# Optimization experiments

Measured on AMD Instinct MI355X. Metric: run time of the kernel, lower is better.

## Reference

```python
import jax, jax.numpy as jnp
import numpy as np
import math

N_HEADS = 8
EMB = 128
KEY_DIM = EMB // N_HEADS  # 16
B, NQ, T = 32, 1024, 1024


def _uniform(key, shape, stdv):
    return jax.random.uniform(key, shape, jnp.float32, -stdv, stdv)


def setup_inputs() -> dict:
    key = jax.random.key(0)
    ks = jax.random.split(key, 7)
    stdv = 1.0 / math.sqrt(KEY_DIM)      # last dim of w_query/w_key/w_value
    stdv_o = 1.0 / math.sqrt(EMB)        # last dim of w_out
    q = jax.random.normal(ks[0], (B, NQ, EMB), jnp.float32)
    h = jax.random.normal(ks[1], (B, T, EMB), jnp.float32)
    mask = jax.random.randint(ks[2], (B, NQ, T), 0, 2).astype(bool)
    return {
        "q": q,
        "h": h,
        "mask": mask,
        "w_query": _uniform(ks[3], (N_HEADS, EMB, KEY_DIM), stdv),
        "w_key": _uniform(ks[4], (N_HEADS, EMB, KEY_DIM), stdv),
        "w_value": _uniform(ks[5], (N_HEADS, EMB, KEY_DIM), stdv),
        "w_out": _uniform(ks[6], (N_HEADS, KEY_DIM, EMB), stdv_o),
    }


def reference(q, h, mask, w_query, w_key, w_value, w_out):
    # q: [B, NQ, E], h: [B, T, E], mask: [B, NQ, T] (True = blocked)
    scale = 1.0 / math.sqrt(KEY_DIM)
    Q = jnp.einsum('bqi,hik->hbqk', q, w_query)   # [H,B,NQ,dk]
    K = jnp.einsum('bti,hik->hbtk', h, w_key)     # [H,B,T,dk]
    V = jnp.einsum('bti,hiv->hbtv', h, w_value)   # [H,B,T,dv]
    U = scale * jnp.einsum('hbqk,hbtk->hbqt', Q, K)  # [H,B,NQ,T]
    m = mask[None]                                   # broadcast over heads
    U = jnp.where(m, -jnp.inf, U)
    attn = jax.nn.softmax(U, axis=-1)
    attn = jnp.where(m, 0.0, attn)                   # explicit zeroing as in original
    heads = jnp.einsum('hbqt,hbtv->hbqv', attn, V)   # [H,B,NQ,dv]
    out = jnp.einsum('hbqv,hve->bqe', heads, w_out)  # [B,NQ,E]
    return out
```

## Files before the change

kernel.cpp:

```cpp
#include <hip/hip_runtime.h>
#include <hip/hip_bf16.h>
#include <stdint.h>


typedef __attribute__((ext_vector_type(8))) short bf16x8;
typedef __attribute__((ext_vector_type(4))) float f32x4;
typedef __attribute__((ext_vector_type(16))) float f32x16;

#define NEGBIG (-1e30f)
#define QSCALE 0.36067376022224085f
#define EXP2(x) __builtin_amdgcn_exp2f(x)
#define PSTRIDE 68

__device__ __forceinline__ unsigned short f2bf(float x) {
  union { __hip_bfloat16 h; unsigned short u; } cv;
  cv.h = __float2bfloat16(x);
  return cv.u;
}
__device__ __forceinline__ unsigned int pk2bf(float a, float b) {
  unsigned int ua = __float_as_uint(a) + 0x8000u;
  unsigned int ub = __float_as_uint(b) + 0x8000u;
  return __builtin_amdgcn_perm(ub, ua, 0x07060302u);
}
__device__ __forceinline__ unsigned int pk2bf_t(float a, float b) {
  return __builtin_amdgcn_perm(__float_as_uint(b), __float_as_uint(a), 0x07060302u);
}

__global__ __launch_bounds__(256) void projmask_k(const float* __restrict__ qp,
                                                  const float* __restrict__ hp,
                                                  const float* __restrict__ wqp,
                                                  const float* __restrict__ wkp,
                                                  const float* __restrict__ wvp,
                                                  const void* __restrict__ mask,
                                                  unsigned short* __restrict__ Qb,
                                                  unsigned short* __restrict__ Kb,
                                                  unsigned short* __restrict__ Vt,
                                                  unsigned long long* __restrict__ mp64) {
  __shared__ unsigned short WtLds[128 * 136];
  __shared__ __align__(16) unsigned short Cxf[9216];
  const int tid = threadIdx.x;

  if (blockIdx.x >= 1536) {
    const int bx = blockIdx.x - 1536;
    unsigned short* mlds = WtLds;
    const unsigned int* mi = (const unsigned int*)mask;
    unsigned int accv = 0;
    #pragma unroll
    for (int k = 0; k < 16; ++k) accv |= mi[k * 251];
    const bool bytemode = accv > 1u;

    const long long i0 = ((long long)bx * 256 + tid) * 16;
    unsigned int v = 0;
    if (bytemode) {
      int4 w = *(const int4*)((const unsigned char*)mask + i0);
      unsigned int ws[4] = {(unsigned)w.x, (unsigned)w.y, (unsigned)w.z, (unsigned)w.w};
      #pragma unroll
      for (int d = 0; d < 4; ++d)
        #pragma unroll
        for (int j = 0; j < 4; ++j)
          v |= (((ws[d] >> (8*j)) & 0xFFu) ? 1u : 0u) << (d*4 + j);
    } else {
      const int4* mp4 = (const int4*)((const int*)mask + i0);
      #pragma unroll
      for (int d = 0; d < 4; ++d) {
        int4 w = mp4[d];
        v |= (w.x ? 1u : 0u) << (d*4 + 0);
        v |= (w.y ? 1u : 0u) << (d*4 + 1);
        v |= (w.z ? 1u : 0u) << (d*4 + 2);
        v |= (w.w ? 1u : 0u) << (d*4 + 3);
      }
    }
    mlds[tid] = (unsigned short)v;
    __syncthreads();
    if (tid < 64)
      mp64[(long long)bx * 64 + tid] = ((const unsigned long long*)mlds)[tid];
    return;
  }

  const int wave = tid >> 6, lane = tid & 63;
  const int llo4 = lane & 15, lhi4 = lane >> 4;
  const int xb = blockIdx.x & 511;
  const int sel = blockIdx.x >> 9;
  const int m0 = xb * 64;
  const int b = m0 >> 10, row0 = m0 & 1023;
  const float* A = (sel == 0) ? qp : hp;
  const float* W = (sel == 0) ? wqp : (sel == 1) ? wkp : wvp;
  const float wscale = (sel == 0) ? QSCALE : 1.0f;

  #pragma unroll
  for (int i = 0; i < 8; ++i) {
    int base = (tid + i * 256) * 8;
    float4 w0 = *(const float4*)&W[base];
    float4 w1 = *(const float4*)&W[base + 4];
    float wv8[8] = {w0.x, w0.y, w0.z, w0.w, w1.x, w1.y, w1.z, w1.w};
    #pragma unroll
    for (int j = 0; j < 8; ++j) {
      int idx = base + j;
      int h = idx >> 11, e = (idx >> 4) & 127, kk = idx & 15;
      WtLds[(h*16 + kk) * 136 + e] = f2bf(wv8[j] * wscale);
    }
  }
  #pragma unroll
  for (int i = 0; i < 4; ++i) {
    int r = (tid >> 4) + i * 16;
    int c = (tid & 15) * 8;
    float4 a0 = *(const float4*)&A[(m0 + r) * 128 + c];
    float4 a1 = *(const float4*)&A[(m0 + r) * 128 + c + 4];
    bf16x8 a8;
    a8[0] = (short)f2bf(a0.x); a8[1] = (short)f2bf(a0.y);
    a8[2] = (short)f2bf(a0.z); a8[3] = (short)f2bf(a0.w);
    a8[4] = (short)f2bf(a1.x); a8[5] = (short)f2bf(a1.y);
    a8[6] = (short)f2bf(a1.z); a8[7] = (short)f2bf(a1.w);
    *(bf16x8*)&Cxf[r * 136 + c] = a8;
  }
  __syncthreads();

  const int n0 = wave * 32;
  f32x4 acc[4][2] = {};
  #pragma unroll
  for (int kk = 0; kk < 128; kk += 32) {
    bf16x8 af[4], bfr[2];
    #pragma unroll
    for (int mi2 = 0; mi2 < 4; ++mi2)
      af[mi2] = *(const bf16x8*)&Cxf[(mi2*16 + llo4)*136 + kk + lhi4*8];
    #pragma unroll
    for (int ni = 0; ni < 2; ++ni)
      bfr[ni] = *(const bf16x8*)&WtLds[(n0 + ni*16 + llo4)*136 + kk + lhi4*8];
    #pragma unroll
    for (int mi2 = 0; mi2 < 4; ++mi2)
      #pragma unroll
      for (int ni = 0; ni < 2; ++ni)
        acc[mi2][ni] = __builtin_amdgcn_mfma_f32_16x16x32_bf16(af[mi2], bfr[ni], acc[mi2][ni], 0, 0, 0);
  }

  __syncthreads();
  if (sel < 2) {
    unsigned short* Cb = sel ? Kb : Qb;
    #pragma unroll
    for (int mi2 = 0; mi2 < 4; ++mi2)
      #pragma unroll
      for (int ni = 0; ni < 2; ++ni) {
        int n = n0 + ni*16 + llo4;
        #pragma unroll
        for (int r = 0; r < 4; ++r)
          Cxf[(mi2*16 + lhi4*4 + r)*136 + n] = f2bf(acc[mi2][ni][r]);
      }
    __syncthreads();
    #pragma unroll
    for (int it = 0; it < 4; ++it) {
      int u = tid + it*256;
      int h = u >> 7, rk = u & 127, row = rk >> 1, kh = rk & 1;
      bf16x8 vv = *(const bf16x8*)&Cxf[row*136 + h*16 + kh*8];
      *(bf16x8*)&Cb[((b*8 + h)*1024 + row0 + row)*16 + kh*8] = vv;
    }
  } else {
    #pragma unroll
    for (int mi2 = 0; mi2 < 4; ++mi2)
      #pragma unroll
      for (int ni = 0; ni < 2; ++ni) {
        int n = n0 + ni*16 + llo4;
        ushort4 pk;
        pk.x = f2bf(acc[mi2][ni][0]); pk.y = f2bf(acc[mi2][ni][1]);
        pk.z = f2bf(acc[mi2][ni][2]); pk.w = f2bf(acc[mi2][ni][3]);
        *(ushort4*)&Cxf[n*72 + mi2*16 + lhi4*4] = pk;
      }
    __syncthreads();
    #pragma unroll
    for (int it = 0; it < 4; ++it) {
      int u = tid + it*256;
      int n = u >> 3, tc = u & 7;
      int h = n >> 4, k = n & 15;
      bf16x8 vv = *(const bf16x8*)&Cxf[n*72 + tc*8];
      *(bf16x8*)&Vt[((b*8 + h)*16 + k)*1024 + row0 + tc*8] = vv;
    }
  }
}

__global__ __launch_bounds__(64) void attn_k(const unsigned short* __restrict__ Qb,
                                             const unsigned short* __restrict__ Kb,
                                             const unsigned short* __restrict__ Vtb,
                                             const unsigned long long* __restrict__ mp64,
                                             unsigned short* __restrict__ heads) {
  __shared__ __align__(16) unsigned short Pw[32 * PSTRIDE];
  __shared__ __align__(8) uint2 mlut[16];
  const int lane = threadIdx.x;
  const int llo4 = lane & 15, lhi4 = lane >> 4;
  const int llo5 = lane & 31, lhi5 = lane >> 5;
  const int q0 = blockIdx.x * 32;
  const int b  = blockIdx.y;
  const int h  = blockIdx.z;
  const int bh = b * 8 + h;
  const unsigned long long* mp_base = &mp64[((b << 10) + q0 + llo5) * 16];
  const unsigned short* Kbase = &Kb[(bh * 1024 + llo5) * 16 + lhi5 * 8];
  const unsigned short* Vbase = &Vtb[(bh * 16 + llo4) * 1024 + lhi4 * 8];

  if (lane < 16) {
    unsigned int n = lane;
    unsigned int h0 = (n & 1u) ? 0u : 0xFFFFu;
    unsigned int h1 = (n & 2u) ? 0u : 0xFFFFu;
    unsigned int h2 = (n & 4u) ? 0u : 0xFFFFu;
    unsigned int h3 = (n & 8u) ? 0u : 0xFFFFu;
    mlut[lane] = make_uint2(h0 | (h1 << 16), h2 | (h3 << 16));
  }

  bf16x8 qf = *(const bf16x8*)&Qb[(bh * 1024 + q0 + llo5) * 16 + lhi5 * 8];

  bf16x8 ones;
  #pragma unroll
  for (int j = 0; j < 8; ++j) ones[j] = (short)0x3F80;
  f32x16 cb16;
  #pragma unroll
  for (int j = 0; j < 16; ++j) cb16[j] = -18.f;

  f32x4 ot[2] = {};
  f32x4 lacc[2] = {};

  bf16x8 kfb[2][2], vfb[2][2];
  unsigned long long mwb[2];

  #pragma unroll
  for (int tt = 0; tt < 2; ++tt)
    kfb[0][tt] = *(const bf16x8*)&Kbase[(tt*32) * 16];
  #pragma unroll
  for (int kt = 0; kt < 2; ++kt)
    vfb[0][kt] = *(const bf16x8*)&Vbase[kt*32];
  mwb[0] = mp_base[0];

  #pragma unroll 2
  for (int tw = 0; tw < 16; ++tw) {
    const int cur = tw & 1, nxt = cur ^ 1;
    const int twn = (tw < 15) ? tw + 1 : 15;
    const int t0n = twn * 64;
    #pragma unroll
    for (int tt = 0; tt < 2; ++tt)
      kfb[nxt][tt] = *(const bf16x8*)&Kbase[(t0n + tt*32) * 16];
    #pragma unroll
    for (int kt = 0; kt < 2; ++kt)
      vfb[nxt][kt] = *(const bf16x8*)&Vbase[t0n + kt*32];
    mwb[nxt] = mp_base[twn];

    f32x16 st[2];
    #pragma unroll
    for (int tt = 0; tt < 2; ++tt)
      st[tt] = __builtin_amdgcn_mfma_f32_32x32x16_bf16(kfb[cur][tt], qf, cb16, 0, 0, 0);

    const unsigned int mwlo = (unsigned int)mwb[cur];
    const unsigned int mwhi = (unsigned int)(mwb[cur] >> 32);
    #pragma unroll
    for (int tt = 0; tt < 2; ++tt) {
      const unsigned int m32 = (tt ? mwhi : mwlo) >> (lhi5 * 4);
      #pragma unroll
      for (int g = 0; g < 4; ++g) {
        unsigned int nib = (m32 >> (g*8)) & 0xFu;
        uint2 am = mlut[nib];
        uint2 d;
        d.x = pk2bf_t(EXP2(st[tt][g*4 + 0]), EXP2(st[tt][g*4 + 1])) & am.x;
        d.y = pk2bf_t(EXP2(st[tt][g*4 + 2]), EXP2(st[tt][g*4 + 3])) & am.y;
        *(uint2*)&Pw[llo5 * PSTRIDE + tt*32 + lhi5*4 + g*8] = d;
      }
    }

    #pragma unroll
    for (int kt = 0; kt < 2; ++kt) {
      #pragma unroll
      for (int qn = 0; qn < 2; ++qn) {
        const unsigned short* pp = &Pw[(qn*16 + llo4) * PSTRIDE + kt*32 + lhi4*8];
        uint2 p0 = *(const uint2*)pp;
        uint2 p1 = *(const uint2*)(pp + 4);
        union { uint2 u[2]; bf16x8 v; } pf;
        pf.u[0] = p0; pf.u[1] = p1;
        ot[qn]   = __builtin_amdgcn_mfma_f32_16x16x32_bf16(vfb[cur][kt], pf.v, ot[qn], 0, 0, 0);
        lacc[qn] = __builtin_amdgcn_mfma_f32_16x16x32_bf16(ones,        pf.v, lacc[qn], 0, 0, 0);
      }
    }
  }

  #pragma unroll
  for (int qn = 0; qn < 2; ++qn) {
    float l = lacc[qn][0];
    float inv = l > 0.f ? 1.f / l : 0.f;
    f32x4 o = ot[qn] * inv;
    uint2 d;
    d.x = pk2bf(o[0], o[1]);
    d.y = pk2bf(o[2], o[3]);
    *(uint2*)&heads[((b << 10) + q0 + qn*16 + llo4) * 128 + h*16 + lhi4*4] = d;
  }
}

__global__ __launch_bounds__(256) void outproj_k(const unsigned short* __restrict__ Av,
                                                 const float* __restrict__ W,
                                                 float* __restrict__ Co) {
  __shared__ unsigned short WtLds[128 * 136];
  __shared__ __align__(16) unsigned short Cxf[9216];
  const int tid = threadIdx.x;
  const int wave = tid >> 6, lane = tid & 63;
  const int llo4 = lane & 15, lhi4 = lane >> 4;
  const int m0 = blockIdx.x * 64;

  #pragma unroll
  for (int i = 0; i < 8; ++i) {
    int base = (tid + i * 256) * 8;
    float4 w0 = *(const float4*)&W[base];
    float4 w1 = *(const float4*)&W[base + 4];
    float wv8[8] = {w0.x, w0.y, w0.z, w0.w, w1.x, w1.y, w1.z, w1.w};
    #pragma unroll
    for (int j = 0; j < 8; ++j) {
      int idx = base + j;
      WtLds[(idx & 127) * 136 + (idx >> 7)] = f2bf(wv8[j]);
    }
  }
  #pragma unroll
  for (int i = 0; i < 4; ++i) {
    int r = (tid >> 4) + i * 16;
    int c = (tid & 15) * 8;
    *(bf16x8*)&Cxf[r * 136 + c] = *(const bf16x8*)&Av[(m0 + r) * 128 + c];
  }
  __syncthreads();

  const int n0 = wave * 32;
  f32x4 acc[4][2] = {};
  #pragma unroll
  for (int kk = 0; kk < 128; kk += 32) {
    bf16x8 af[4], bfr[2];
    #pragma unroll
    for (int mi2 = 0; mi2 < 4; ++mi2)
      af[mi2] = *(const bf16x8*)&Cxf[(mi2*16 + llo4)*136 + kk + lhi4*8];
    #pragma unroll
    for (int ni = 0; ni < 2; ++ni)
      bfr[ni] = *(const bf16x8*)&WtLds[(n0 + ni*16 + llo4)*136 + kk + lhi4*8];
    #pragma unroll
    for (int mi2 = 0; mi2 < 4; ++mi2)
      #pragma unroll
      for (int ni = 0; ni < 2; ++ni)
        acc[mi2][ni] = __builtin_amdgcn_mfma_f32_16x16x32_bf16(af[mi2], bfr[ni], acc[mi2][ni], 0, 0, 0);
  }
  #pragma unroll
  for (int mi2 = 0; mi2 < 4; ++mi2)
    #pragma unroll
    for (int ni = 0; ni < 2; ++ni) {
      int n = n0 + ni*16 + llo4;
      int mbase = m0 + mi2*16 + lhi4*4;
      #pragma unroll
      for (int r = 0; r < 4; ++r)
        Co[(mbase + r) * 128 + n] = acc[mi2][ni][r];
    }
}

extern "C" void kernel_launch(void* const* d_in, const int* in_sizes, int n_in,
                              void* d_out, int out_size, void* d_ws, size_t ws_size,
                              hipStream_t stream) {
  const float* q  = (const float*)d_in[0];
  const float* hh = (const float*)d_in[1];
  const void*  mk = d_in[2];
  const float* wq = (const float*)d_in[3];
  const float* wk = (const float*)d_in[4];
  const float* wv = (const float*)d_in[5];
  const float* wo = (const float*)d_in[6];
  float* out = (float*)d_out;

  unsigned short* Qb = (unsigned short*)d_ws;
  unsigned short* Kb = Qb + 32*8*1024*16;
  unsigned short* Vt = Kb + 32*8*1024*16;
  unsigned short* hd = Vt + 32*8*1024*16;
  unsigned long long* mp64 = (unsigned long long*)(hd + 32768*128);

  projmask_k<<<9728, 256, 0, stream>>>(q, hh, wq, wk, wv, mk, Qb, Kb, Vt, mp64);
  attn_k<<<dim3(32, 32, 8), 64, 0, stream>>>(Qb, Kb, Vt, mp64, hd);
  outproj_k<<<512, 256, 0, stream>>>(hd, wo, out);
}
```

Measured before the change: 301.8 us.

## Keep P in registers via lane shuffles and fuse row-sum into 32x32 PV MFMA

The attention kernel no longer stages the probability tile through shared memory. P fragments from the QK^T 32x32 MFMA output are rearranged across half-waves with shuffles into the B-operand layout of a 32x32x16 MFMA. The V operand is padded with rows of ones, so the softmax denominator comes out of the same accumulator and the separate ones-MFMA is gone. The -18 bias accumulator initialisation is dropped (zero init), which changes the exp2 offset and could overflow for large scores. V loads are no longer prefetched one iteration ahead.

Measured after the change: 307.9 us. 2.0% more time.

```diff
diff --git a/kernel.cpp b/kernel.cpp
--- a/kernel.cpp
+++ b/kernel.cpp
@@ -7,10 +7,8 @@
 typedef __attribute__((ext_vector_type(4))) float f32x4;
 typedef __attribute__((ext_vector_type(16))) float f32x16;
 
-#define NEGBIG (-1e30f)
 #define QSCALE 0.36067376022224085f
 #define EXP2(x) __builtin_amdgcn_exp2f(x)
-#define PSTRIDE 68
 
 __device__ __forceinline__ unsigned short f2bf(float x) {
   union { __hip_bfloat16 h; unsigned short u; } cv;
@@ -181,10 +179,8 @@
                                              const unsigned short* __restrict__ Vtb,
                                              const unsigned long long* __restrict__ mp64,
                                              unsigned short* __restrict__ heads) {
-  __shared__ __align__(16) unsigned short Pw[32 * PSTRIDE];
   __shared__ __align__(8) uint2 mlut[16];
   const int lane = threadIdx.x;
-  const int llo4 = lane & 15, lhi4 = lane >> 4;
   const int llo5 = lane & 31, lhi5 = lane >> 5;
   const int q0 = blockIdx.x * 32;
   const int b  = blockIdx.y;
@@ -192,7 +188,7 @@
   const int bh = b * 8 + h;
   const unsigned long long* mp_base = &mp64[((b << 10) + q0 + llo5) * 16];
   const unsigned short* Kbase = &Kb[(bh * 1024 + llo5) * 16 + lhi5 * 8];
-  const unsigned short* Vbase = &Vtb[(bh * 16 + llo4) * 1024 + lhi4 * 8];
+  const unsigned short* Vbase = &Vtb[(bh * 16 + (llo5 & 15)) * 1024 + lhi5 * 8];
 
   if (lane < 16) {
     unsigned int n = lane;
@@ -205,86 +201,82 @@
 
   bf16x8 qf = *(const bf16x8*)&Qb[(bh * 1024 + q0 + llo5) * 16 + lhi5 * 8];
 
-  bf16x8 ones;
-  #pragma unroll
-  for (int j = 0; j < 8; ++j) ones[j] = (short)0x3F80;
-  f32x16 cb16;
-  #pragma unroll
-  for (int j = 0; j < 16; ++j) cb16[j] = -18.f;
-
-  f32x4 ot[2] = {};
-  f32x4 lacc[2] = {};
-
-  bf16x8 kfb[2][2], vfb[2][2];
+  bf16x8 ones8;
+  #pragma unroll
+  for (int j = 0; j < 8; ++j) ones8[j] = (short)0x3F80;
+  const f32x16 z16 = {};
+
+  f32x16 acc = {};
+
+  bf16x8 kfb[2][2];
   unsigned long long mwb[2];
 
   #pragma unroll
   for (int tt = 0; tt < 2; ++tt)
     kfb[0][tt] = *(const bf16x8*)&Kbase[(tt*32) * 16];
-  #pragma unroll
-  for (int kt = 0; kt < 2; ++kt)
-    vfb[0][kt] = *(const bf16x8*)&Vbase[kt*32];
   mwb[0] = mp_base[0];
 
   #pragma unroll 2
   for (int tw = 0; tw < 16; ++tw) {
     const int cur = tw & 1, nxt = cur ^ 1;
     const int twn = (tw < 15) ? tw + 1 : 15;
-    const int t0n = twn * 64;
+    const int t0  = tw * 64;
     #pragma unroll
     for (int tt = 0; tt < 2; ++tt)
-      kfb[nxt][tt] = *(const bf16x8*)&Kbase[(t0n + tt*32) * 16];
-    #pragma unroll
-    for (int kt = 0; kt < 2; ++kt)
-      vfb[nxt][kt] = *(const bf16x8*)&Vbase[t0n + kt*32];
+      kfb[nxt][tt] = *(const bf16x8*)&Kbase[(twn*64 + tt*32) * 16];
     mwb[nxt] = mp_base[twn];
 
+    bf16x8 vs[4];
+    #pragma unroll
+    for (int s = 0; s < 4; ++s) {
+      vs[s] = ones8;
+      if (llo5 < 16)
+        vs[s] = *(const bf16x8*)&Vbase[t0 + s*16];
+    }
+
     f32x16 st[2];
     #pragma unroll
-    for (int tt = 0; tt < 2; ++tt)
-      st[tt] = __builtin_amdgcn_mfma_f32_32x32x16_bf16(kfb[cur][tt], qf, cb16, 0, 0, 0);
+    for (int tt = 0; tt < 2; ++tt) {
+      st[tt] = __builtin_amdgcn_mfma_f32_32x32x16_bf16(kfb[cur][tt], qf, z16, 0, 0, 0);
+      #pragma unroll
+      for (int r = 0; r < 16; ++r)
+        st[tt][r] = EXP2(st[tt][r]);
+    }
 
     const unsigned int mwlo = (unsigned int)mwb[cur];
     const unsigned int mwhi = (unsigned int)(mwb[cur] >> 32);
     #pragma unroll
-    for (int tt = 0; tt < 2; ++tt) {
+    for (int s = 0; s < 4; ++s) {
+      const int tt = s >> 1, rb = (s & 1) * 8;
       const unsigned int m32 = (tt ? mwhi : mwlo) >> (lhi5 * 4);
-      #pragma unroll
-      for (int g = 0; g < 4; ++g) {
-        unsigned int nib = (m32 >> (g*8)) & 0xFu;
-        uint2 am = mlut[nib];
-        uint2 d;
-        d.x = pk2bf_t(EXP2(st[tt][g*4 + 0]), EXP2(st[tt][g*4 + 1])) & am.x;
-        d.y = pk2bf_t(EXP2(st[tt][g*4 + 2]), EXP2(st[tt][g*4 + 3])) & am.y;
-        *(uint2*)&Pw[llo5 * PSTRIDE + tt*32 + lhi5*4 + g*8] = d;
-      }
-    }
-
-    #pragma unroll
-    for (int kt = 0; kt < 2; ++kt) {
-      #pragma unroll
-      for (int qn = 0; qn < 2; ++qn) {
-        const unsigned short* pp = &Pw[(qn*16 + llo4) * PSTRIDE + kt*32 + lhi4*8];
-        uint2 p0 = *(const uint2*)pp;
-        uint2 p1 = *(const uint2*)(pp + 4);
-        union { uint2 u[2]; bf16x8 v; } pf;
-        pf.u[0] = p0; pf.u[1] = p1;
-        ot[qn]   = __builtin_amdgcn_mfma_f32_16x16x32_bf16(vfb[cur][kt], pf.v, ot[qn], 0, 0, 0);
-        lacc[qn] = __builtin_amdgcn_mfma_f32_16x16x32_bf16(ones,        pf.v, lacc[qn], 0, 0, 0);
-      }
-    }
-  }
-
-  #pragma unroll
-  for (int qn = 0; qn < 2; ++qn) {
-    float l = lacc[qn][0];
-    float inv = l > 0.f ? 1.f / l : 0.f;
-    f32x4 o = ot[qn] * inv;
-    uint2 d;
-    d.x = pk2bf(o[0], o[1]);
-    d.y = pk2bf(o[2], o[3]);
-    *(uint2*)&heads[((b << 10) + q0 + qn*16 + llo4) * 128 + h*16 + lhi4*4] = d;
-  }
+      const int g0 = (s & 1) * 2;
+      uint2 amA = mlut[(m32 >> (g0*8)) & 0xFu];
+      uint2 amB = mlut[(m32 >> (g0*8 + 8)) & 0xFu];
+      unsigned int A = pk2bf_t(st[tt][rb+0], st[tt][rb+1]) & amA.x;
+      unsigned int Bq = pk2bf_t(st[tt][rb+2], st[tt][rb+3]) & amA.y;
+      unsigned int C = pk2bf_t(st[tt][rb+4], st[tt][rb+5]) & amB.x;
+      unsigned int D = pk2bf_t(st[tt][rb+6], st[tt][rb+7]) & amB.y;
+      unsigned int Y1 = __shfl_xor(lhi5 ? A : C, 32);
+      unsigned int Y2 = __shfl_xor(lhi5 ? Bq : D, 32);
+      union { unsigned int u[4]; bf16x8 v; } pf;
+      pf.u[0] = lhi5 ? Y1 : A;
+      pf.u[1] = lhi5 ? Y2 : Bq;
+      pf.u[2] = lhi5 ? C  : Y1;
+      pf.u[3] = lhi5 ? D  : Y2;
+      acc = __builtin_amdgcn_mfma_f32_32x32x16_bf16(vs[s], pf.v, acc, 0, 0, 0);
+    }
+  }
+
+  float l = acc[8];
+  float inv = l > 0.f ? 1.f / l : 0.f;
+  unsigned short* hp2 = &heads[((b << 10) + q0 + llo5) * 128 + h*16];
+  uint2 d0, d1;
+  d0.x = pk2bf(acc[0]*inv, acc[1]*inv);
+  d0.y = pk2bf(acc[2]*inv, acc[3]*inv);
+  d1.x = pk2bf(acc[4]*inv, acc[5]*inv);
+  d1.y = pk2bf(acc[6]*inv, acc[7]*inv);
+  *(uint2*)&hp2[4*lhi5]     = d0;
+  *(uint2*)&hp2[8 + 4*lhi5] = d1;
 }
 
 __global__ __launch_bounds__(256) void outproj_k(const unsigned short* __restrict__ Av,
```
